# Optimization experiments

Hardware: AMD Instinct MI355X
Metric: run time of the kernel (lower is better)

## Reference

```python
import jax, jax.numpy as jnp
import numpy as np

D_MODEL = 1024
N_HEADS = 16
HEAD_DIM = D_MODEL // N_HEADS


def alibi_slopes(n_heads):
    # power-of-2 case: m_i = (2^(-8/n))^i for i=1..n
    base = 2.0 ** (-8.0 / n_heads)
    return jnp.asarray([base ** i for i in range(1, n_heads + 1)], dtype=jnp.float32)


def setup_inputs() -> dict:
    key = jax.random.key(0)
    kx, kq, kk, kv, ko = jax.random.split(key, 5)
    B, T = 2, 2048
    scale = 0.02
    x = jax.random.normal(kx, (B, T, D_MODEL), dtype=jnp.float32)
    Wq = jax.random.normal(kq, (D_MODEL, D_MODEL), dtype=jnp.float32) * scale
    Wk = jax.random.normal(kk, (D_MODEL, D_MODEL), dtype=jnp.float32) * scale
    Wv = jax.random.normal(kv, (D_MODEL, D_MODEL), dtype=jnp.float32) * scale
    Wo = jax.random.normal(ko, (D_MODEL, D_MODEL), dtype=jnp.float32) * scale
    return {"x": x, "Wq": Wq, "Wk": Wk, "Wv": Wv, "Wo": Wo}


def reference(x, Wq, Wk, Wv, Wo):
    B, T, D = x.shape
    H, hd = N_HEADS, HEAD_DIM
    # projections (torch Linear: x @ W.T), split into heads -> (B,H,T,hd)
    def proj(W):
        return (x @ W.T).reshape(B, T, H, hd).transpose(0, 2, 1, 3)
    q, k, v = proj(Wq), proj(Wk), proj(Wv)
    scale = hd ** -0.5
    scores = jnp.einsum('bhqd,bhkd->bhqk', q, k) * scale  # (B,H,T,T)
    # ALiBi causal bias: -slope * |i-j| on causal positions, 0 on future
    pos = jnp.arange(T, dtype=jnp.float32)
    dist = jnp.abs(pos[:, None] - pos[None, :])  # (T,T)
    causal = pos[:, None] >= pos[None, :]        # (T,T) bool, j <= i
    slopes = alibi_slopes(H)
    bias = -slopes[:, None, None] * jnp.where(causal, dist, 0.0)  # (H,T,T)
    scores = scores + bias[None]
    scores = jnp.where(causal[None, None], scores, -jnp.inf)
    attn = jax.nn.softmax(scores, axis=-1)
    out = jnp.einsum('bhqk,bhkd->bhqd', attn, v)  # (B,H,T,hd)
    out = out.transpose(0, 2, 1, 3).reshape(B, T, D)
    return out @ Wo.T
```

## Files before the change

kernel.cpp:

```cpp
#include <hip/hip_runtime.h>
#include <math.h>


#define T_SEQ 2048
#define DM    1024
#define NH    16
#define HD    64
#define NROW  4096

typedef __attribute__((ext_vector_type(8))) short bf16x8;
typedef __attribute__((ext_vector_type(4))) short bf16x4;
typedef __attribute__((ext_vector_type(4))) float f32x4;

__device__ __forceinline__ short f2bf(float f) {
  unsigned u = __float_as_uint(f);
  u += 0x7FFFu + ((u >> 16) & 1u);
  return (short)(u >> 16);
}

__device__ __forceinline__ void gload_lds16(short* lds, const short* g) {
  __builtin_amdgcn_global_load_lds((const __attribute__((address_space(1))) void*)g,
                                   (__attribute__((address_space(3))) void*)lds, 16, 0, 0);
}

__global__ __launch_bounds__(256) void convert_all(
    const float* __restrict__ x,  const float* __restrict__ wq,
    const float* __restrict__ wk, const float* __restrict__ wv,
    const float* __restrict__ wo,
    short* __restrict__ xb,  short* __restrict__ wqb, short* __restrict__ wkb,
    short* __restrict__ wvb, short* __restrict__ wob) {
  const int i = blockIdx.x * 256 + threadIdx.x;
  const float* s; short* d; int off;
  if (i < (1 << 20)) { s = x; d = xb; off = i; }
  else {
    const int j = i - (1 << 20);
    const int w = j >> 18;
    off = j & ((1 << 18) - 1);
    s = (w == 0) ? wq : (w == 1) ? wk : (w == 2) ? wv : wo;
    d = (w == 0) ? wqb : (w == 1) ? wkb : (w == 2) ? wvb : wob;
  }
  const float4 v = ((const float4*)s)[off];
  bf16x4 o = {f2bf(v.x), f2bf(v.y), f2bf(v.z), f2bf(v.w)};
  *(bf16x4*)(d + 4 * (size_t)off) = o;
}

template <typename OutT>
__device__ __forceinline__ void gemm_body(const short* __restrict__ A,
                                          const short* __restrict__ W,
                                          OutT* __restrict__ C) {
  __shared__ short sA[128][32];
  __shared__ short sB[128][32];
  const int tid  = threadIdx.x;
  const int lane = tid & 63, wv = tid >> 6;
  const int quad = lane >> 4, l16 = lane & 15;
  const int wm = (wv >> 1) * 64, wn = (wv & 1) * 64;
  const size_t m0 = (size_t)blockIdx.x * 128, n0 = (size_t)blockIdx.y * 128;

  f32x4 acc[4][4];
#pragma unroll
  for (int i = 0; i < 4; ++i)
#pragma unroll
    for (int j = 0; j < 4; ++j) acc[i][j] = (f32x4){0.f, 0.f, 0.f, 0.f};

  const int grow = lane >> 2;
  const int gcol = (lane & 3) << 3;

  for (int k0 = 0; k0 < DM; k0 += 32) {
    __syncthreads();
    {
      const short* ga = A + (m0 + wv * 32 + grow) * DM + k0 + gcol;
      gload_lds16(&sA[wv * 32][0],      ga);
      gload_lds16(&sA[wv * 32 + 16][0], ga + 16 * DM);
      const short* gb = W + (n0 + wv * 32 + grow) * DM + k0 + gcol;
      gload_lds16(&sB[wv * 32][0],      gb);
      gload_lds16(&sB[wv * 32 + 16][0], gb + 16 * DM);
    }
    __syncthreads();

    bf16x8 af[4], bfr[4];
#pragma unroll
    for (int t = 0; t < 4; ++t) {
      af[t]  = *(const bf16x8*)&sA[wm + t * 16 + l16][quad * 8];
      bfr[t] = *(const bf16x8*)&sB[wn + t * 16 + l16][quad * 8];
    }
#pragma unroll
    for (int mt = 0; mt < 4; ++mt)
#pragma unroll
      for (int nt = 0; nt < 4; ++nt)
        acc[mt][nt] = __builtin_amdgcn_mfma_f32_16x16x32_bf16(af[mt], bfr[nt], acc[mt][nt], 0, 0, 0);
  }
#pragma unroll
  for (int mt = 0; mt < 4; ++mt) {
#pragma unroll
    for (int r = 0; r < 4; ++r) {
      const size_t m = m0 + wm + mt * 16 + quad * 4 + r;
      OutT* crow = C + m * DM;
#pragma unroll
      for (int nt = 0; nt < 4; ++nt) {
        const float v = acc[mt][nt][r];
        if constexpr (sizeof(OutT) == 2)
          crow[n0 + wn + nt * 16 + l16] = f2bf(v);
        else
          crow[n0 + wn + nt * 16 + l16] = v;
      }
    }
  }
}

__global__ __launch_bounds__(256) void gemm_qkv(
    const short* __restrict__ x,
    const short* __restrict__ Wq, const short* __restrict__ Wk, const short* __restrict__ Wv,
    short* __restrict__ Qb, short* __restrict__ Kb, short* __restrict__ Vb) {
  const short* W = (blockIdx.z == 0) ? Wq : (blockIdx.z == 1) ? Wk : Wv;
  short*       C = (blockIdx.z == 0) ? Qb : (blockIdx.z == 1) ? Kb : Vb;
  gemm_body<short>(x, W, C);
}

__global__ __launch_bounds__(256) void gemm_out(const short* __restrict__ A,
                                                const short* __restrict__ W,
                                                float* __restrict__ C) {
  gemm_body<float>(A, W, C);
}

__global__ __launch_bounds__(256) void flash_alibi(const short* __restrict__ Q,
                                                   const short* __restrict__ K,
                                                   const short* __restrict__ V,
                                                   short* __restrict__ O) {
  __shared__ short sK[64][72];
  __shared__ unsigned int sVt2[64][34];
  __shared__ short sP[4][16][72];

  const int tid  = threadIdx.x;
  const int lane = tid & 63, wv = tid >> 6;
  const int quad = lane >> 4, l16 = lane & 15;
  const int qt = (int)gridDim.x - 1 - (int)blockIdx.x;
  const int h = blockIdx.y, b = blockIdx.z;
  const size_t base = (size_t)b * T_SEQ * DM + (size_t)h * HD;
  const int qi_base = qt * 64;

  bf16x8 qf[2];
  {
    const int qrow = qi_base + wv * 16 + l16;
    const short* qp = Q + base + (size_t)qrow * DM + quad * 8;
    qf[0] = *(const bf16x8*)(qp);
    qf[1] = *(const bf16x8*)(qp + 32);
  }

  const float slope = exp2f(-0.5f * (float)(h + 1));
  const int srow = tid >> 3;
  const int scol = (tid & 7) << 3;
  const int kpair = tid >> 3;
  const int d0 = (tid & 7) << 3;

  f32x4 oacc[4];
#pragma unroll
  for (int c = 0; c < 4; ++c) oacc[c] = (f32x4){0.f, 0.f, 0.f, 0.f};
  float lpart[4] = {0.f, 0.f, 0.f, 0.f};

  for (int kt = 0; kt <= qt; ++kt) {
    const int k0 = kt * 64;
    __syncthreads();
#pragma unroll
    for (int p = 0; p < 2; ++p) {
      const int row = srow + p * 32;
      *(bf16x8*)&sK[row][scol] = *(const bf16x8*)(K + base + (size_t)(k0 + row) * DM + scol);
    }
    {
      const short* v0 = V + base + (size_t)(k0 + 2 * kpair) * DM + d0;
      bf16x8 va = *(const bf16x8*)v0;
      bf16x8 vb = *(const bf16x8*)(v0 + DM);
#pragma unroll
      for (int e = 0; e < 8; ++e) {
        unsigned w = ((unsigned)(unsigned short)va[e]) |
                     (((unsigned)(unsigned short)vb[e]) << 16);
        sVt2[d0 + e][kpair] = w;
      }
    }
    __syncthreads();

    f32x4 sacc[4];
#pragma unroll
    for (int c = 0; c < 4; ++c) {
      f32x4 a = (f32x4){0.f, 0.f, 0.f, 0.f};
      a = __builtin_amdgcn_mfma_f32_16x16x32_bf16(
              qf[0], *(const bf16x8*)&sK[c * 16 + l16][quad * 8], a, 0, 0, 0);
      a = __builtin_amdgcn_mfma_f32_16x16x32_bf16(
              qf[1], *(const bf16x8*)&sK[c * 16 + l16][32 + quad * 8], a, 0, 0, 0);
      sacc[c] = a;
    }

#pragma unroll
    for (int r = 0; r < 4; ++r) {
      const int qi = qi_base + wv * 16 + quad * 4 + r;
#pragma unroll
      for (int c = 0; c < 4; ++c) {
        const int kj = k0 + c * 16 + l16;
        float p = 0.0f;
        if (kj <= qi)
          p = __expf(sacc[c][r] * 0.125f - slope * (float)(qi - kj) - 12.0f);
        lpart[r] += p;
        sP[wv][quad * 4 + r][c * 16 + l16] = f2bf(p);
      }
    }

#pragma unroll
    for (int s = 0; s < 2; ++s) {
      bf16x8 pf = *(const bf16x8*)&sP[wv][l16][s * 32 + quad * 8];
#pragma unroll
      for (int c = 0; c < 4; ++c) {
        const unsigned* vp = &sVt2[c * 16 + l16][s * 16 + quad * 4];
        bf16x4 vlo = *(const bf16x4*)vp;
        bf16x4 vhi = *(const bf16x4*)(vp + 2);
        bf16x8 vf = {vlo[0], vlo[1], vlo[2], vlo[3], vhi[0], vhi[1], vhi[2], vhi[3]};
        oacc[c] = __builtin_amdgcn_mfma_f32_16x16x32_bf16(pf, vf, oacc[c], 0, 0, 0);
      }
    }
  }

#pragma unroll
  for (int r = 0; r < 4; ++r) {
    float l = lpart[r];
#pragma unroll
    for (int off = 1; off < 16; off <<= 1) l += __shfl_xor(l, off);
    const float inv = 1.0f / fmaxf(l, 1e-37f);
    const int qi = qi_base + wv * 16 + quad * 4 + r;
    short* orow = O + base + (size_t)qi * DM;
#pragma unroll
    for (int c = 0; c < 4; ++c)
      orow[c * 16 + l16] = f2bf(oacc[c][r] * inv);
  }
}

extern "C" void kernel_launch(void* const* d_in, const int* in_sizes, int n_in,
                              void* d_out, int out_size, void* d_ws, size_t ws_size,
                              hipStream_t stream) {
  float* out = (float*)d_out;

  short* ws = (short*)d_ws;
  const size_t plane = (size_t)NROW * DM;
  const size_t wsz   = (size_t)DM * DM;
  short* xb  = ws;
  short* Wqb = xb + plane;
  short* Wkb = Wqb + wsz;
  short* Wvb = Wkb + wsz;
  short* Wob = Wvb + wsz;
  short* Qb  = Wob + wsz;
  short* Kb  = Qb + plane;
  short* Vb  = Kb + plane;
  short* Ab  = Vb + plane;

  dim3 blk(256);
  convert_all<<<8192, blk, 0, stream>>>(
      (const float*)d_in[0], (const float*)d_in[1], (const float*)d_in[2],
      (const float*)d_in[3], (const float*)d_in[4],
      xb, Wqb, Wkb, Wvb, Wob);

  gemm_qkv<<<dim3(NROW / 128, DM / 128, 3), blk, 0, stream>>>(xb, Wqb, Wkb, Wvb, Qb, Kb, Vb);
  flash_alibi<<<dim3(T_SEQ / 64, NH, 2), blk, 0, stream>>>(Qb, Kb, Vb, Ab);
  gemm_out<<<dim3(NROW / 128, DM / 128, 1), blk, 0, stream>>>(Ab, Wob, out);
}
```

Before: 229.3 us.

## Pair causal query tiles per block, widen GEMM K-tile, streamline softmax exp

The attention kernel now gives each block two query tiles, tile i and tile 31-i. Every block then does the same amount of causal work, and each K/V tile loaded into shared memory is reused by both query tiles, with half as many blocks launched. The softmax exponent moves to exp2 with the ALiBi terms precomputed per row and column. The masking branch only runs on the diagonal tile, and P is converted to bf16 by truncation instead of rounding. The GEMMs stage 64-wide K slices so there are half as many barrier pairs, and the LDS paddings change; the costs are more registers, less parallelism in attention, and slightly lower precision from truncating P.

```diff
diff --git a/kernel.cpp b/kernel.cpp
--- a/kernel.cpp
+++ b/kernel.cpp
@@ -48,8 +48,8 @@
 __device__ __forceinline__ void gemm_body(const short* __restrict__ A,
                                           const short* __restrict__ W,
                                           OutT* __restrict__ C) {
-  __shared__ short sA[128][32];
-  __shared__ short sB[128][32];
+  __shared__ short sA[128][64];
+  __shared__ short sB[128][64];
   const int tid  = threadIdx.x;
   const int lane = tid & 63, wv = tid >> 6;
   const int quad = lane >> 4, l16 = lane & 15;
@@ -62,32 +62,34 @@
 #pragma unroll
     for (int j = 0; j < 4; ++j) acc[i][j] = (f32x4){0.f, 0.f, 0.f, 0.f};
 
-  const int grow = lane >> 2;
-  const int gcol = (lane & 3) << 3;
-
-  for (int k0 = 0; k0 < DM; k0 += 32) {
-    __syncthreads();
-    {
-      const short* ga = A + (m0 + wv * 32 + grow) * DM + k0 + gcol;
-      gload_lds16(&sA[wv * 32][0],      ga);
-      gload_lds16(&sA[wv * 32 + 16][0], ga + 16 * DM);
-      const short* gb = W + (n0 + wv * 32 + grow) * DM + k0 + gcol;
-      gload_lds16(&sB[wv * 32][0],      gb);
-      gload_lds16(&sB[wv * 32 + 16][0], gb + 16 * DM);
-    }
-    __syncthreads();
-
-    bf16x8 af[4], bfr[4];
-#pragma unroll
-    for (int t = 0; t < 4; ++t) {
-      af[t]  = *(const bf16x8*)&sA[wm + t * 16 + l16][quad * 8];
-      bfr[t] = *(const bf16x8*)&sB[wn + t * 16 + l16][quad * 8];
-    }
-#pragma unroll
-    for (int mt = 0; mt < 4; ++mt)
-#pragma unroll
-      for (int nt = 0; nt < 4; ++nt)
-        acc[mt][nt] = __builtin_amdgcn_mfma_f32_16x16x32_bf16(af[mt], bfr[nt], acc[mt][nt], 0, 0, 0);
+  const int grow = lane >> 3;
+  const int gcol = (lane & 7) << 3;
+
+  for (int k0 = 0; k0 < DM; k0 += 64) {
+    __syncthreads();
+#pragma unroll
+    for (int j = 0; j < 4; ++j) {
+      gload_lds16(&sA[wv * 32 + j * 8][0],
+                  A + (m0 + wv * 32 + j * 8 + grow) * DM + k0 + gcol);
+      gload_lds16(&sB[wv * 32 + j * 8][0],
+                  W + (n0 + wv * 32 + j * 8 + grow) * DM + k0 + gcol);
+    }
+    __syncthreads();
+
+#pragma unroll
+    for (int kk = 0; kk < 64; kk += 32) {
+      bf16x8 af[4], bfr[4];
+#pragma unroll
+      for (int t = 0; t < 4; ++t) {
+        af[t]  = *(const bf16x8*)&sA[wm + t * 16 + l16][kk + quad * 8];
+        bfr[t] = *(const bf16x8*)&sB[wn + t * 16 + l16][kk + quad * 8];
+      }
+#pragma unroll
+      for (int mt = 0; mt < 4; ++mt)
+#pragma unroll
+        for (int nt = 0; nt < 4; ++nt)
+          acc[mt][nt] = __builtin_amdgcn_mfma_f32_16x16x32_bf16(af[mt], bfr[nt], acc[mt][nt], 0, 0, 0);
+    }
   }
 #pragma unroll
   for (int mt = 0; mt < 4; ++mt) {
@@ -127,38 +129,60 @@
                                                    const short* __restrict__ V,
                                                    short* __restrict__ O) {
   __shared__ short sK[64][72];
-  __shared__ unsigned int sVt2[64][34];
-  __shared__ short sP[4][16][72];
+  __shared__ unsigned int sVt2[64][35];
+  __shared__ short sP[4][16][76];
 
   const int tid  = threadIdx.x;
   const int lane = tid & 63, wv = tid >> 6;
   const int quad = lane >> 4, l16 = lane & 15;
-  const int qt = (int)gridDim.x - 1 - (int)blockIdx.x;
+  const int qtA = blockIdx.x;
+  const int qtB = 31 - qtA;
   const int h = blockIdx.y, b = blockIdx.z;
   const size_t base = (size_t)b * T_SEQ * DM + (size_t)h * HD;
-  const int qi_base = qt * 64;
-
-  bf16x8 qf[2];
+
+  const int qiA0 = qtA * 64 + wv * 16;
+  const int qiB0 = qtB * 64 + wv * 16;
+
+  bf16x8 qfA[2], qfB[2];
   {
-    const int qrow = qi_base + wv * 16 + l16;
-    const short* qp = Q + base + (size_t)qrow * DM + quad * 8;
-    qf[0] = *(const bf16x8*)(qp);
-    qf[1] = *(const bf16x8*)(qp + 32);
-  }
-
+    const short* qa = Q + base + (size_t)(qiA0 + l16) * DM + quad * 8;
+    qfA[0] = *(const bf16x8*)(qa);
+    qfA[1] = *(const bf16x8*)(qa + 32);
+    const short* qb = Q + base + (size_t)(qiB0 + l16) * DM + quad * 8;
+    qfB[0] = *(const bf16x8*)(qb);
+    qfB[1] = *(const bf16x8*)(qb + 32);
+  }
+
+  const float L2E = 1.4426950408889634f;
   const float slope = exp2f(-0.5f * (float)(h + 1));
+  const float sl2 = slope * L2E;
+  const float SC = 0.125f * L2E;
+
+  float kcol[4], qrowA[4], qrowB[4];
+#pragma unroll
+  for (int c = 0; c < 4; ++c) kcol[c] = sl2 * (float)(c * 16 + l16);
+#pragma unroll
+  for (int r = 0; r < 4; ++r) {
+    qrowA[r] = sl2 * (float)(qiA0 + quad * 4 + r) + 12.0f * L2E;
+    qrowB[r] = sl2 * (float)(qiB0 + quad * 4 + r) + 12.0f * L2E;
+  }
+
+  f32x4 oaccA[4], oaccB[4];
+#pragma unroll
+  for (int c = 0; c < 4; ++c) {
+    oaccA[c] = (f32x4){0.f, 0.f, 0.f, 0.f};
+    oaccB[c] = (f32x4){0.f, 0.f, 0.f, 0.f};
+  }
+  float lpartA[4] = {0.f, 0.f, 0.f, 0.f};
+  float lpartB[4] = {0.f, 0.f, 0.f, 0.f};
+
   const int srow = tid >> 3;
   const int scol = (tid & 7) << 3;
   const int kpair = tid >> 3;
   const int d0 = (tid & 7) << 3;
 
-  f32x4 oacc[4];
-#pragma unroll
-  for (int c = 0; c < 4; ++c) oacc[c] = (f32x4){0.f, 0.f, 0.f, 0.f};
-  float lpart[4] = {0.f, 0.f, 0.f, 0.f};
-
-  for (int kt = 0; kt <= qt; ++kt) {
-    const int k0 = kt * 64;
+  int k0 = 0;
+  for (int kt = 0; kt <= qtB; ++kt, k0 += 64) {
     __syncthreads();
 #pragma unroll
     for (int p = 0; p < 2; ++p) {
@@ -178,56 +202,70 @@
     }
     __syncthreads();
 
-    f32x4 sacc[4];
+    const float t0 = sl2 * (float)k0;
+
+    auto compute = [&](const bf16x8* qf, f32x4* oacc, float* lpart,
+                       const float* qrow, int qi0, bool mask) {
+      f32x4 sacc[4];
+#pragma unroll
+      for (int c = 0; c < 4; ++c) {
+        f32x4 a = (f32x4){0.f, 0.f, 0.f, 0.f};
+        a = __builtin_amdgcn_mfma_f32_16x16x32_bf16(
+                qf[0], *(const bf16x8*)&sK[c * 16 + l16][quad * 8], a, 0, 0, 0);
+        a = __builtin_amdgcn_mfma_f32_16x16x32_bf16(
+                qf[1], *(const bf16x8*)&sK[c * 16 + l16][32 + quad * 8], a, 0, 0, 0);
+        sacc[c] = a;
+      }
+#pragma unroll
+      for (int c = 0; c < 4; ++c) {
+        const float tc = t0 + kcol[c];
+#pragma unroll
+        for (int r = 0; r < 4; ++r) {
+          float p = exp2f(fmaf(sacc[c][r], SC, tc - qrow[r]));
+          if (mask) {
+            const int kj = k0 + c * 16 + l16;
+            const int qi = qi0 + quad * 4 + r;
+            p = (kj <= qi) ? p : 0.0f;
+          }
+          lpart[r] += p;
+          sP[wv][quad * 4 + r][c * 16 + l16] = (short)(__float_as_uint(p) >> 16);
+        }
+      }
+#pragma unroll
+      for (int s = 0; s < 2; ++s) {
+        bf16x8 pf = *(const bf16x8*)&sP[wv][l16][s * 32 + quad * 8];
+#pragma unroll
+        for (int c = 0; c < 4; ++c) {
+          const unsigned* vp = &sVt2[c * 16 + l16][s * 16 + quad * 4];
+          bf16x4 vlo = *(const bf16x4*)vp;
+          bf16x4 vhi = *(const bf16x4*)(vp + 2);
+          bf16x8 vf = {vlo[0], vlo[1], vlo[2], vlo[3], vhi[0], vhi[1], vhi[2], vhi[3]};
+          oacc[c] = __builtin_amdgcn_mfma_f32_16x16x32_bf16(pf, vf, oacc[c], 0, 0, 0);
+        }
+      }
+    };
+
+    compute(qfB, oaccB, lpartB, qrowB, qiB0, kt == qtB);
+    if (kt <= qtA) compute(qfA, oaccA, lpartA, qrowA, qiA0, kt == qtA);
+  }
+
+#pragma unroll
+  for (int r = 0; r < 4; ++r) {
+    float lA = lpartA[r], lB = lpartB[r];
+#pragma unroll
+    for (int off = 1; off < 16; off <<= 1) {
+      lA += __shfl_xor(lA, off);
+      lB += __shfl_xor(lB, off);
+    }
+    const float invA = 1.0f / fmaxf(lA, 1e-37f);
+    const float invB = 1.0f / fmaxf(lB, 1e-37f);
+    short* orowA = O + base + (size_t)(qiA0 + quad * 4 + r) * DM;
+    short* orowB = O + base + (size_t)(qiB0 + quad * 4 + r) * DM;
 #pragma unroll
     for (int c = 0; c < 4; ++c) {
-      f32x4 a = (f32x4){0.f, 0.f, 0.f, 0.f};
-      a = __builtin_amdgcn_mfma_f32_16x16x32_bf16(
-              qf[0], *(const bf16x8*)&sK[c * 16 + l16][quad * 8], a, 0, 0, 0);
-      a = __builtin_amdgcn_mfma_f32_16x16x32_bf16(
-              qf[1], *(const bf16x8*)&sK[c * 16 + l16][32 + quad * 8], a, 0, 0, 0);
-      sacc[c] = a;
-    }
-
-#pragma unroll
-    for (int r = 0; r < 4; ++r) {
-      const int qi = qi_base + wv * 16 + quad * 4 + r;
-#pragma unroll
-      for (int c = 0; c < 4; ++c) {
-        const int kj = k0 + c * 16 + l16;
-        float p = 0.0f;
-        if (kj <= qi)
-          p = __expf(sacc[c][r] * 0.125f - slope * (float)(qi - kj) - 12.0f);
-        lpart[r] += p;
-        sP[wv][quad * 4 + r][c * 16 + l16] = f2bf(p);
-      }
-    }
-
-#pragma unroll
-    for (int s = 0; s < 2; ++s) {
-      bf16x8 pf = *(const bf16x8*)&sP[wv][l16][s * 32 + quad * 8];
-#pragma unroll
-      for (int c = 0; c < 4; ++c) {
-        const unsigned* vp = &sVt2[c * 16 + l16][s * 16 + quad * 4];
-        bf16x4 vlo = *(const bf16x4*)vp;
-        bf16x4 vhi = *(const bf16x4*)(vp + 2);
-        bf16x8 vf = {vlo[0], vlo[1], vlo[2], vlo[3], vhi[0], vhi[1], vhi[2], vhi[3]};
-        oacc[c] = __builtin_amdgcn_mfma_f32_16x16x32_bf16(pf, vf, oacc[c], 0, 0, 0);
-      }
-    }
-  }
-
-#pragma unroll
-  for (int r = 0; r < 4; ++r) {
-    float l = lpart[r];
-#pragma unroll
-    for (int off = 1; off < 16; off <<= 1) l += __shfl_xor(l, off);
-    const float inv = 1.0f / fmaxf(l, 1e-37f);
-    const int qi = qi_base + wv * 16 + quad * 4 + r;
-    short* orow = O + base + (size_t)qi * DM;
-#pragma unroll
-    for (int c = 0; c < 4; ++c)
-      orow[c * 16 + l16] = f2bf(oacc[c][r] * inv);
+      orowA[c * 16 + l16] = f2bf(oaccA[c][r] * invA);
+      orowB[c * 16 + l16] = f2bf(oaccB[c][r] * invB);
+    }
   }
 }
 
@@ -256,6 +294,6 @@
       xb, Wqb, Wkb, Wvb, Wob);
 
   gemm_qkv<<<dim3(NROW / 128, DM / 128, 3), blk, 0, stream>>>(xb, Wqb, Wkb, Wvb, Qb, Kb, Vb);
-  flash_alibi<<<dim3(T_SEQ / 64, NH, 2), blk, 0, stream>>>(Qb, Kb, Vb, Ab);
+  flash_alibi<<<dim3(T_SEQ / 128, NH, 2), blk, 0, stream>>>(Qb, Kb, Vb, Ab);
   gemm_out<<<dim3(NROW / 128, DM / 128, 1), blk, 0, stream>>>(Ab, Wob, out);
 }
```

New measurement: 308.3 us. 34.5% more time.

## Split long causal query tiles across two blocks and combine partials

Applied to the files above, without the earlier changes.

The upper 16 query tiles are split into two KV-range halves (split-K) so the attention grid has more, better-balanced work items. Each half writes unnormalized bf16 partial outputs and row sums, and a new combine kernel merges them. The exp math is also reformulated with exp2 and precomputed per-row/per-column bias terms, the causal mask is applied only on the diagonal tile, P is truncated rather than rounded to bf16, and the LDS padding is changed. The extra combine launch and partial-buffer traffic add cost, and storing partials in bf16 loses some precision.

```diff
diff --git a/kernel.cpp b/kernel.cpp
--- a/kernel.cpp
+++ b/kernel.cpp
@@ -16,6 +16,9 @@
   unsigned u = __float_as_uint(f);
   u += 0x7FFFu + ((u >> 16) & 1u);
   return (short)(u >> 16);
+}
+__device__ __forceinline__ float bf2f(short s) {
+  return __uint_as_float(((unsigned)(unsigned short)s) << 16);
 }
 
 __device__ __forceinline__ void gload_lds16(short* lds, const short* g) {
@@ -125,39 +128,60 @@
 __global__ __launch_bounds__(256) void flash_alibi(const short* __restrict__ Q,
                                                    const short* __restrict__ K,
                                                    const short* __restrict__ V,
-                                                   short* __restrict__ O) {
+                                                   short* __restrict__ O,
+                                                   short* __restrict__ Po,
+                                                   float* __restrict__ Pl) {
   __shared__ short sK[64][72];
-  __shared__ unsigned int sVt2[64][34];
-  __shared__ short sP[4][16][72];
+  __shared__ unsigned int sVt2[64][35];
+  __shared__ short sP[4][16][76];
 
   const int tid  = threadIdx.x;
   const int lane = tid & 63, wv = tid >> 6;
   const int quad = lane >> 4, l16 = lane & 15;
-  const int qt = (int)gridDim.x - 1 - (int)blockIdx.x;
+  const int item = blockIdx.x;
+  int qt, half;
+  if (item < 32) { qt = 16 + (item >> 1); half = item & 1; }
+  else           { qt = 47 - item;        half = -1; }
+  const int n = qt + 1;
+  int kts, kte;
+  if (half < 0) { kts = 0; kte = n; }
+  else { const int n0 = n >> 1; kts = half ? n0 : 0; kte = half ? n : n0; }
+
   const int h = blockIdx.y, b = blockIdx.z;
   const size_t base = (size_t)b * T_SEQ * DM + (size_t)h * HD;
   const int qi_base = qt * 64;
+  const int qi0 = qi_base + wv * 16;
 
   bf16x8 qf[2];
   {
-    const int qrow = qi_base + wv * 16 + l16;
-    const short* qp = Q + base + (size_t)qrow * DM + quad * 8;
+    const short* qp = Q + base + (size_t)(qi0 + l16) * DM + quad * 8;
     qf[0] = *(const bf16x8*)(qp);
     qf[1] = *(const bf16x8*)(qp + 32);
   }
 
+  const float L2E = 1.4426950408889634f;
   const float slope = exp2f(-0.5f * (float)(h + 1));
+  const float sl2 = slope * L2E;
+  const float SC = 0.125f * L2E;
+
+  float kcol[4], qrow[4];
+#pragma unroll
+  for (int c = 0; c < 4; ++c) kcol[c] = sl2 * (float)(c * 16 + l16);
+#pragma unroll
+  for (int r = 0; r < 4; ++r)
+    qrow[r] = sl2 * (float)(qi0 + quad * 4 + r) + 12.0f * L2E;
+
+  f32x4 oacc[4];
+#pragma unroll
+  for (int c = 0; c < 4; ++c) oacc[c] = (f32x4){0.f, 0.f, 0.f, 0.f};
+  float lpart[4] = {0.f, 0.f, 0.f, 0.f};
+
   const int srow = tid >> 3;
   const int scol = (tid & 7) << 3;
   const int kpair = tid >> 3;
   const int d0 = (tid & 7) << 3;
 
-  f32x4 oacc[4];
-#pragma unroll
-  for (int c = 0; c < 4; ++c) oacc[c] = (f32x4){0.f, 0.f, 0.f, 0.f};
-  float lpart[4] = {0.f, 0.f, 0.f, 0.f};
-
-  for (int kt = 0; kt <= qt; ++kt) {
+  for (int kt = kts; kt < kte; ++kt) {
     const int k0 = kt * 64;
     __syncthreads();
 #pragma unroll
@@ -189,17 +213,21 @@
       sacc[c] = a;
     }
 
-#pragma unroll
-    for (int r = 0; r < 4; ++r) {
-      const int qi = qi_base + wv * 16 + quad * 4 + r;
-#pragma unroll
-      for (int c = 0; c < 4; ++c) {
-        const int kj = k0 + c * 16 + l16;
-        float p = 0.0f;
-        if (kj <= qi)
-          p = __expf(sacc[c][r] * 0.125f - slope * (float)(qi - kj) - 12.0f);
+    const float t0 = sl2 * (float)k0;
+    const bool mask = (kt == qt);
+#pragma unroll
+    for (int c = 0; c < 4; ++c) {
+      const float tc = t0 + kcol[c];
+#pragma unroll
+      for (int r = 0; r < 4; ++r) {
+        float p = exp2f(fmaf(sacc[c][r], SC, tc - qrow[r]));
+        if (mask) {
+          const int kj = k0 + c * 16 + l16;
+          const int qi = qi0 + quad * 4 + r;
+          p = (kj <= qi) ? p : 0.0f;
+        }
         lpart[r] += p;
-        sP[wv][quad * 4 + r][c * 16 + l16] = f2bf(p);
+        sP[wv][quad * 4 + r][c * 16 + l16] = (short)(__float_as_uint(p) >> 16);
       }
     }
 
@@ -217,18 +245,58 @@
     }
   }
 
-#pragma unroll
-  for (int r = 0; r < 4; ++r) {
-    float l = lpart[r];
-#pragma unroll
-    for (int off = 1; off < 16; off <<= 1) l += __shfl_xor(l, off);
-    const float inv = 1.0f / fmaxf(l, 1e-37f);
-    const int qi = qi_base + wv * 16 + quad * 4 + r;
-    short* orow = O + base + (size_t)qi * DM;
-#pragma unroll
-    for (int c = 0; c < 4; ++c)
-      orow[c * 16 + l16] = f2bf(oacc[c][r] * inv);
-  }
+  if (half < 0) {
+#pragma unroll
+    for (int r = 0; r < 4; ++r) {
+      float l = lpart[r];
+#pragma unroll
+      for (int off = 1; off < 16; off <<= 1) l += __shfl_xor(l, off);
+      const float inv = 1.0f / fmaxf(l, 1e-37f);
+      short* orow = O + base + (size_t)(qi0 + quad * 4 + r) * DM;
+#pragma unroll
+      for (int c = 0; c < 4; ++c)
+        orow[c * 16 + l16] = f2bf(oacc[c][r] * inv);
+    }
+  } else {
+    const int pidx = (((b * NH + h) * 16) + (qt - 16)) * 2 + half;
+    short* po = Po + (size_t)pidx * 4096;
+    float* pl = Pl + (size_t)pidx * 64;
+#pragma unroll
+    for (int r = 0; r < 4; ++r) {
+      float l = lpart[r];
+#pragma unroll
+      for (int off = 1; off < 16; off <<= 1) l += __shfl_xor(l, off);
+      const int row = wv * 16 + quad * 4 + r;
+      if (l16 == 0) pl[row] = l;
+#pragma unroll
+      for (int c = 0; c < 4; ++c)
+        po[row * 64 + c * 16 + l16] = f2bf(oacc[c][r]);
+    }
+  }
+}
+
+__global__ __launch_bounds__(256) void combine(const short* __restrict__ Po,
+                                               const float* __restrict__ Pl,
+                                               short* __restrict__ O) {
+  const int g = blockIdx.x * 32 + (threadIdx.x >> 3);
+  const int d = (threadIdx.x & 7) << 3;
+  const int row = g & 63;
+  const int lt  = (g >> 6) & 15;
+  const int h   = (g >> 10) & 15;
+  const int b   = g >> 14;
+  const int pbase = (((b * NH + h) * 16) + lt) * 2;
+  const short* p0 = Po + (size_t)(pbase + 0) * 4096 + row * 64 + d;
+  const short* p1 = Po + (size_t)(pbase + 1) * 4096 + row * 64 + d;
+  const float l = Pl[(pbase + 0) * 64 + row] + Pl[(pbase + 1) * 64 + row];
+  const float inv = 1.0f / fmaxf(l, 1e-37f);
+  bf16x8 a = *(const bf16x8*)p0;
+  bf16x8 bb = *(const bf16x8*)p1;
+  const int qi = (16 + lt) * 64 + row;
+  short* orow = O + (size_t)b * T_SEQ * DM + (size_t)qi * DM + h * HD + d;
+  bf16x8 o;
+#pragma unroll
+  for (int e = 0; e < 8; ++e) o[e] = f2bf((bf2f(a[e]) + bf2f(bb[e])) * inv);
+  *(bf16x8*)orow = o;
 }
 
 extern "C" void kernel_launch(void* const* d_in, const int* in_sizes, int n_in,
@@ -248,6 +316,8 @@
   short* Kb  = Qb + plane;
   short* Vb  = Kb + plane;
   short* Ab  = Vb + plane;
+  short* Po  = Ab + plane;
+  float* Pl  = (float*)(Po + (size_t)1024 * 4096);
 
   dim3 blk(256);
   convert_all<<<8192, blk, 0, stream>>>(
@@ -256,6 +326,7 @@
       xb, Wqb, Wkb, Wvb, Wob);
 
   gemm_qkv<<<dim3(NROW / 128, DM / 128, 3), blk, 0, stream>>>(xb, Wqb, Wkb, Wvb, Qb, Kb, Vb);
-  flash_alibi<<<dim3(T_SEQ / 64, NH, 2), blk, 0, stream>>>(Qb, Kb, Vb, Ab);
+  flash_alibi<<<dim3(48, NH, 2), blk, 0, stream>>>(Qb, Kb, Vb, Ab, Po, Pl);
+  combine<<<1024, blk, 0, stream>>>(Po, Pl, Ab);
   gemm_out<<<dim3(NROW / 128, DM / 128, 1), blk, 0, stream>>>(Ab, Wob, out);
 }
```

After: 337.8 us. 47.4% more time.
